# Kernel optimization log

Measured on AMD Instinct MI355X. Metric: run time of the kernel, lower is better.

The kernel has to match this reference:

```python
import jax, jax.numpy as jnp
import numpy as np

PATCH = 16  # SpatialCorrelationSampler patch_size; kernel_size=1, stride=1, dilation_patch=1


def conv3x3(x, w, b):
    # NCHW conv, 3x3, stride 1, padding 1 (matches nn.Conv2d(..., 3, 1, 1))
    y = jax.lax.conv_general_dilated(
        x, w, window_strides=(1, 1), padding=((1, 1), (1, 1)),
        dimension_numbers=('NCHW', 'OIHW', 'NCHW'))
    return y + b[None, :, None, None]


def correlate(f0, f1):
    """SpatialCorrelationSampler(kernel_size=1, patch_size=16, stride=1, padding=0).
    out[b, pi, pj, y, x] = sum_c f0[b,c,y,x] * f1[b,c,y+pi-8, x+pj-8] (zero-padded),
    displacements -8..7 in each axis; no normalization (matches the
    Pytorch-Correlation-extension implementation). Returned flattened to
    [B, PATCH*PATCH, H, W] as the module does via .view."""
    B, C, H, W = f0.shape
    half = PATCH // 2  # 8 -> displacements [-8, 7]
    f1p = jnp.pad(f1, ((0, 0), (0, 0), (half, PATCH - 1 - half), (half, PATCH - 1 - half)))

    def step(_, d):
        pi, pj = d // PATCH, d % PATCH
        f1s = jax.lax.dynamic_slice(f1p, (0, 0, pi, pj), (B, C, H, W))
        return None, jnp.sum(f0 * f1s, axis=1)  # [B, H, W]

    _, corr = jax.lax.scan(step, None, jnp.arange(PATCH * PATCH))  # [256, B, H, W]
    return jnp.transpose(corr, (1, 0, 2, 3))  # [B, 256, H, W]


def setup_inputs() -> dict:
    key = jax.random.key(0)
    ks = jax.random.split(key, 4)
    B, C, H, W = 2, 256, 96, 160  # C == FMAP_DIM (forced: C + 256 + C == 3*C)
    hidden = 256
    f_0 = jax.random.normal(ks[0], (B, C, H, W), jnp.float32)
    f_1 = jax.random.normal(ks[1], (B, C, H, W), jnp.float32)
    W1 = jax.random.normal(ks[2], (hidden, 3 * C, 3, 3), jnp.float32) * 0.02
    b1 = jnp.zeros((hidden,), jnp.float32)
    W2 = jax.random.normal(ks[3], (C, hidden, 3, 3), jnp.float32) * 0.02
    b2 = jnp.zeros((C,), jnp.float32)
    return {"f_0": f_0, "f_1": f_1, "W1": W1, "b1": b1, "W2": W2, "b2": b2}


def reference(f_0, f_1, W1, b1, W2, b2):
    corr = correlate(f_0, f_1)                       # [B, 256, H, W]
    f_cat = jnp.concatenate([f_0, corr, f_1], axis=1)  # [B, 3C, H, W]
    h = jax.nn.relu(conv3x3(f_cat, W1, b1))
    f_1_delta = conv3x3(h, W2, b2)
    return f_1 + f_1_delta
```

## Files before the change

### kernel.cpp

```cpp
#include <hip/hip_runtime.h>
#include <stdint.h>

#define NB 2
#define NC 256
#define NH 96
#define NW 160
#define HP 98
#define WP 162
#define CATC 768
#define P8H 112
#define P8W 176

typedef __bf16 bf16x8 __attribute__((ext_vector_type(8)));
typedef float f32x4 __attribute__((ext_vector_type(4)));

static __device__ __forceinline__ uint16_t f2bf(float f) {
  uint32_t u = __float_as_uint(f);
  return (uint16_t)((u + 0x7fffu + ((u >> 16) & 1u)) >> 16);
}

static __device__ __forceinline__ void gload16(const void* g, void* l) {
  __builtin_amdgcn_global_load_lds(
      (const __attribute__((address_space(1))) uint32_t*)g,
      (__attribute__((address_space(3))) uint32_t*)l, 16, 0, 0);
}

__global__ void __launch_bounds__(256) wprep_kernel(const float* __restrict__ wsrc,
                                                    uint16_t* __restrict__ dst, int cin) {
  int co = blockIdx.x;
  int nb = cin >> 5;
  for (int ci = threadIdx.x; ci < cin; ci += 256) {
    const float* s = wsrc + ((size_t)co * cin + ci) * 9;
    int cb = ci >> 5, cil = ci & 31;
#pragma unroll
    for (int t = 0; t < 9; ++t) {
      dst[(((size_t)t * nb + cb) * 256 + co) * 32 + cil] = f2bf(s[t]);
    }
  }
}

__global__ void __launch_bounds__(256) transpose_kernel(const float* __restrict__ f0,
                                                        const float* __restrict__ f1,
                                                        uint16_t* __restrict__ fcat,
                                                        uint16_t* __restrict__ f1p8) {
  __shared__ float tile[32][33];
  int tid = threadIdx.x;
  int tx = tid & 31, ty = tid >> 5;
  int xb = blockIdx.x;
  int y = blockIdx.y;
  int z = blockIdx.z;
  int b = z >> 4, which = (z >> 3) & 1, cb = z & 7;
  const float* src = which ? f1 : f0;
  int x0 = xb * 32;
#pragma unroll
  for (int j = 0; j < 4; ++j) {
    int c = cb * 32 + ty + j * 8;
    tile[ty + j * 8][tx] = src[((size_t)(b * NC + c) * NH + y) * NW + x0 + tx];
  }
  __syncthreads();
#pragma unroll
  for (int j = 0; j < 4; ++j) {
    int lx = ty + j * 8;
    int x = x0 + lx;
    int c = cb * 32 + tx;
    uint16_t v = f2bf(tile[tx][lx]);
    size_t base = ((size_t)(b * HP + y + 1) * WP + (x + 1)) * CATC;
    if (which == 0) {
      fcat[base + c] = v;
    } else {
      fcat[base + 512 + c] = v;
      f1p8[((size_t)(b * P8H + y + 8) * P8W + (x + 8)) * NC + c] = v;
    }
  }
}

__global__ void __launch_bounds__(256) corr_kernel(const uint16_t* __restrict__ fcat,
                                                   const uint16_t* __restrict__ f1p8,
                                                   uint16_t* __restrict__ fout) {
  int tid = threadIdx.x;
  int lane = tid & 63, w = tid >> 6;
  int lr = lane & 15, lk = lane >> 4;
  int lin = blockIdx.x;
  int wid = (lin & 7) * 120 + (lin >> 3);
  int y = wid % 96, xt = wid / 96;
  int b = blockIdx.y;
  int x0 = xt * 16;

  bf16x8 af[8];
  const uint16_t* abase = fcat + ((size_t)(b * HP + y + 1) * WP + (x0 + lr + 1)) * CATC + lk * 8;
#pragma unroll
  for (int kk = 0; kk < 8; ++kk) af[kk] = *(const bf16x8*)(abase + kk * 32);

  for (int g = 0; g < 4; ++g) {
    int pi = g * 4 + w;
    const uint16_t* bbase =
        f1p8 + ((size_t)(b * P8H + y + pi) * P8W + x0) * NC + lk * 8;
    bf16x8 bf0[8], bf1[8];
#pragma unroll
    for (int kk = 0; kk < 8; ++kk) {
      bf0[kk] = *(const bf16x8*)(bbase + (size_t)lr * NC + kk * 32);
      bf1[kk] = *(const bf16x8*)(bbase + (size_t)(16 + lr) * NC + kk * 32);
    }
    f32x4 acc0 = (f32x4){0.f, 0.f, 0.f, 0.f};
    f32x4 acc1 = (f32x4){0.f, 0.f, 0.f, 0.f};
#pragma unroll
    for (int kk = 0; kk < 8; ++kk) {
      acc0 = __builtin_amdgcn_mfma_f32_16x16x32_bf16(af[kk], bf0[kk], acc0, 0, 0, 0);
      acc1 = __builtin_amdgcn_mfma_f32_16x16x32_bf16(af[kk], bf1[kk], acc1, 0, 0, 0);
    }
    size_t orow = ((size_t)(b * HP + y + 1) * WP + (x0 + 1)) * CATC + 256 + (size_t)pi * 16;
#pragma unroll
    for (int j = 0; j < 4; ++j) {
      int xl = lk * 4 + j;
      int pj0 = lr - xl;
      if (pj0 >= 0) fout[orow + (size_t)xl * CATC + pj0] = f2bf(acc0[j]);
      int pj1 = 16 + lr - xl;
      if (pj1 < 16) fout[orow + (size_t)xl * CATC + pj1] = f2bf(acc1[j]);
    }
  }
}

__global__ __launch_bounds__(512, 2) void conv1_kernel(const uint16_t* __restrict__ fcat,
                                                       const uint16_t* __restrict__ wp,
                                                       const float* __restrict__ bias,
                                                       uint16_t* __restrict__ hbuf) {
  constexpr int CBS = 24, NT = 9 * CBS;
  __shared__ __align__(16) uint16_t As[3][128 * 32];
  int tid = threadIdx.x;
  int w = tid >> 6, lane = tid & 63;
  int lr = lane & 15, lk = lane >> 4;
  int wr = w >> 2, wc = w & 3;

  int orig = blockIdx.x;
  int swz = (orig & 7) * 30 + (orig >> 3);
  int b = swz / 120, rem = swz % 120;
  int xt = rem / 12, yt = rem % 12;
  int x0 = xt * 16, y0 = yt * 8;

  int sr = w * 16 + (lane >> 2);
  int scp = lane & 3;
  int sy = y0 + (sr >> 4), sx = x0 + (sr & 15);
  uint16_t* lds0 = &As[0][0] + sr * 32 + scp * 8;

  float bv[4];
#pragma unroll
  for (int n = 0; n < 4; ++n) bv[n] = bias[wc * 64 + n * 16 + lr];

  f32x4 acc[4][4];
#pragma unroll
  for (int m = 0; m < 4; ++m)
#pragma unroll
    for (int n = 0; n < 4; ++n) acc[m][n] = (f32x4){0.f, 0.f, 0.f, 0.f};

#define STAGE1(kt, buf)                                                                   \
  {                                                                                       \
    int t_ = (kt) / CBS, cb_ = (kt) - t_ * CBS;                                           \
    int dy_ = t_ / 3, dx_ = t_ - dy_ * 3;                                                 \
    const uint16_t* g_ =                                                                  \
        fcat + ((size_t)(b * HP + sy + dy_) * WP + (sx + dx_)) * CATC + cb_ * 32 + scp * 8; \
    gload16(g_, lds0 + (buf)*4096);                                                       \
  }

#define LOADB1(dst, kt)                                                       \
  {                                                                           \
    const uint16_t* s_ = wp + ((size_t)(kt)*256 + wc * 64 + lr) * 32 + lk * 8; \
    _Pragma("unroll") for (int n_ = 0; n_ < 4; ++n_) dst[n_] =                \
        *(const bf16x8*)(s_ + (size_t)n_ * 16 * 32);                          \
  }

  bf16x8 bcur[4], bnext[4];
  STAGE1(0, 0);
  STAGE1(1, 1);
  LOADB1(bcur, 0);
  asm volatile("s_waitcnt vmcnt(5)" ::: "memory");
  __builtin_amdgcn_s_barrier();

  for (int kt = 0; kt < NT; ++kt) {
    int nkt = kt + 2 < NT ? kt + 2 : NT - 1;
    STAGE1(nkt, (kt + 2) % 3);
    int bkt = kt + 1 < NT ? kt + 1 : NT - 1;
    LOADB1(bnext, bkt);
    const uint16_t* a = &As[kt % 3][0];
    bf16x8 af[4];
#pragma unroll
    for (int m = 0; m < 4; ++m)
      af[m] = *(const bf16x8*)(a + (wr * 64 + m * 16 + lr) * 32 + lk * 8);
#pragma unroll
    for (int m = 0; m < 4; ++m)
#pragma unroll
      for (int n = 0; n < 4; ++n)
        acc[m][n] = __builtin_amdgcn_mfma_f32_16x16x32_bf16(af[m], bcur[n], acc[m][n], 0, 0, 0);
#pragma unroll
    for (int n = 0; n < 4; ++n) bcur[n] = bnext[n];
    asm volatile("s_waitcnt vmcnt(5)" ::: "memory");
    __builtin_amdgcn_s_barrier();
  }

#pragma unroll
  for (int m = 0; m < 4; ++m) {
#pragma unroll
    for (int j = 0; j < 4; ++j) {
      int px = wr * 64 + m * 16 + lk * 4 + j;
      int py = px >> 4, pxx = px & 15;
      size_t base = ((size_t)(b * HP + y0 + py + 1) * WP + (x0 + pxx + 1)) * NC;
#pragma unroll
      for (int n = 0; n < 4; ++n) {
        float v = acc[m][n][j] + bv[n];
        v = v > 0.f ? v : 0.f;
        hbuf[base + wc * 64 + n * 16 + lr] = f2bf(v);
      }
    }
  }
#undef STAGE1
#undef LOADB1
}

__global__ __launch_bounds__(512, 2) void conv2_kernel(const uint16_t* __restrict__ hbuf,
                                                       const uint16_t* __restrict__ wp,
                                                       const float* __restrict__ bias,
                                                       const float* __restrict__ f1,
                                                       float* __restrict__ out) {
  constexpr int CBS = 8, NT = 72;
  __shared__ __align__(16) uint16_t Ws[3][256 * 32];
  int tid = threadIdx.x;
  int w = tid >> 6, lane = tid & 63;
  int lr = lane & 15, lk = lane >> 4;
  int wq = w & 3;
  int wph = w >> 2;

  int orig = blockIdx.x;
  int swz = (orig & 7) * 30 + (orig >> 3);
  int b = swz / 120, rem = swz % 120;
  int xt = rem / 12, yt = rem % 12;
  int x0 = xt * 16, y0 = yt * 8;

  int scp = lane & 3;

  float bv[4][4];
#pragma unroll
  for (int m = 0; m < 4; ++m)
#pragma unroll
    for (int j = 0; j < 4; ++j) bv[m][j] = bias[wq * 64 + m * 16 + lk * 4 + j];

  f32x4 acc[4][4];
#pragma unroll
  for (int m = 0; m < 4; ++m)
#pragma unroll
    for (int n = 0; n < 4; ++n) acc[m][n] = (f32x4){0.f, 0.f, 0.f, 0.f};

#define STAGE2(kt, buf)                                                        \
  {                                                                            \
    const uint16_t* g_ = wp + ((size_t)(kt)*256) * 32;                         \
    _Pragma("unroll") for (int j_ = 0; j_ < 2; ++j_) {                         \
      int r_ = w * 32 + j_ * 16 + (lane >> 2);                                 \
      gload16(g_ + r_ * 32 + scp * 8, &Ws[buf][0] + r_ * 32 + scp * 8);        \
    }                                                                          \
  }

#define LOADX2(dst, kt)                                                                     \
  {                                                                                         \
    int t_ = (kt) >> 3, cb_ = (kt)&7;                                                       \
    int dy_ = t_ / 3, dx_ = t_ - dy_ * 3;                                                   \
    _Pragma("unroll") for (int n_ = 0; n_ < 4; ++n_) {                                      \
      const uint16_t* g_ = hbuf +                                                           \
          ((size_t)(b * HP + y0 + wph * 4 + n_ + dy_) * WP + (x0 + lr + dx_)) * NC +        \
          cb_ * 32 + lk * 8;                                                                \
      dst[n_] = *(const bf16x8*)g_;                                                         \
    }                                                                                       \
  }

  bf16x8 xcur[4], xnext[4];
  STAGE2(0, 0);
  STAGE2(1, 1);
  LOADX2(xcur, 0);
  asm volatile("s_waitcnt vmcnt(6)" ::: "memory");
  __builtin_amdgcn_s_barrier();

  for (int kt = 0; kt < NT; ++kt) {
    int nkt = kt + 2 < NT ? kt + 2 : NT - 1;
    STAGE2(nkt, (kt + 2) % 3);
    int bkt = kt + 1 < NT ? kt + 1 : NT - 1;
    LOADX2(xnext, bkt);
    const uint16_t* a = &Ws[kt % 3][0];
    bf16x8 af[4];
#pragma unroll
    for (int m = 0; m < 4; ++m)
      af[m] = *(const bf16x8*)(a + (wq * 64 + m * 16 + lr) * 32 + lk * 8);
#pragma unroll
    for (int m = 0; m < 4; ++m)
#pragma unroll
      for (int n = 0; n < 4; ++n)
        acc[m][n] = __builtin_amdgcn_mfma_f32_16x16x32_bf16(af[m], xcur[n], acc[m][n], 0, 0, 0);
#pragma unroll
    for (int n = 0; n < 4; ++n) xcur[n] = xnext[n];
    asm volatile("s_waitcnt vmcnt(6)" ::: "memory");
    __builtin_amdgcn_s_barrier();
  }

#pragma unroll
  for (int m = 0; m < 4; ++m) {
#pragma unroll
    for (int j = 0; j < 4; ++j) {
      int co = wq * 64 + m * 16 + lk * 4 + j;
#pragma unroll
      for (int n = 0; n < 4; ++n) {
        int y = y0 + wph * 4 + n;
        size_t idx = ((size_t)(b * NC + co) * NH + y) * NW + x0 + lr;
        out[idx] = acc[m][n][j] + bv[m][j] + f1[idx];
      }
    }
  }
#undef STAGE2
#undef LOADX2
}

extern "C" void kernel_launch(void* const* d_in, const int* in_sizes, int n_in,
                              void* d_out, int out_size, void* d_ws, size_t ws_size,
                              hipStream_t stream) {
  (void)in_sizes; (void)n_in; (void)out_size; (void)ws_size;
  const float* f0 = (const float*)d_in[0];
  const float* f1 = (const float*)d_in[1];
  const float* W1 = (const float*)d_in[2];
  const float* b1 = (const float*)d_in[3];
  const float* W2 = (const float*)d_in[4];
  const float* b2 = (const float*)d_in[5];
  float* out = (float*)d_out;

  char* ws = (char*)d_ws;
  size_t s_fcat = (size_t)NB * HP * WP * CATC * 2;
  size_t s_f1p8 = (size_t)NB * P8H * P8W * NC * 2;
  size_t s_h = (size_t)NB * HP * WP * NC * 2;
  size_t s_bp1 = (size_t)9 * 24 * 256 * 32 * 2;
  uint16_t* fcat = (uint16_t*)ws;
  uint16_t* f1p8 = (uint16_t*)(ws + s_fcat);
  uint16_t* hbuf = (uint16_t*)(ws + s_fcat + s_f1p8);
  uint16_t* bp1 = (uint16_t*)(ws + s_fcat + s_f1p8 + s_h);
  uint16_t* bp2 = (uint16_t*)(ws + s_fcat + s_f1p8 + s_h + s_bp1);

  hipMemsetAsync(fcat, 0, s_fcat, stream);
  hipMemsetAsync(f1p8, 0, s_f1p8, stream);
  hipMemsetAsync(hbuf, 0, s_h, stream);

  wprep_kernel<<<256, 256, 0, stream>>>(W1, bp1, 768);
  wprep_kernel<<<256, 256, 0, stream>>>(W2, bp2, 256);
  transpose_kernel<<<dim3(5, 96, 32), 256, 0, stream>>>(f0, f1, fcat, f1p8);
  corr_kernel<<<dim3(960, 2), 256, 0, stream>>>(fcat, f1p8, fcat);
  conv1_kernel<<<240, 512, 0, stream>>>(fcat, bp1, b1, hbuf);
  conv2_kernel<<<240, 512, 0, stream>>>(hbuf, bp2, b2, f1, out);
}
```

Measured before the change: 432.7 us.

## XOR-swizzle LDS tiles and double-buffer register operands in both conv GEMMs

Both implicit-GEMM conv kernels now store their shared-memory tiles with an XOR swizzle on the 16-byte chunk index. The global source address is permuted and the fragment reads use the matching swizzled offset, which is meant to cut LDS bank conflicts on the bf16x8 loads. The main loops are unrolled by two with two alternating register buffers for the directly loaded operand, and each step computes on the current stage before issuing the next loads. This removes the per-iteration register copies, but issuing loads after the MFMAs may hide less memory latency, and the prologue now waits for all outstanding loads.

Measured after the change: 427.5 us. No clear change (-1.2%).

```diff
diff --git a/kernel.cpp b/kernel.cpp
--- a/kernel.cpp
+++ b/kernel.cpp
@@ -139,8 +139,10 @@
 
   int sr = w * 16 + (lane >> 2);
   int scp = lane & 3;
+  int cg = scp ^ ((sr >> 1) & 3);
   int sy = y0 + (sr >> 4), sx = x0 + (sr & 15);
   uint16_t* lds0 = &As[0][0] + sr * 32 + scp * 8;
+  int cswz = (lk ^ ((lr >> 1) & 3)) * 8;
 
   float bv[4];
 #pragma unroll
@@ -152,48 +154,59 @@
 #pragma unroll
     for (int n = 0; n < 4; ++n) acc[m][n] = (f32x4){0.f, 0.f, 0.f, 0.f};
 
-#define STAGE1(kt, buf)                                                                   \
-  {                                                                                       \
-    int t_ = (kt) / CBS, cb_ = (kt) - t_ * CBS;                                           \
-    int dy_ = t_ / 3, dx_ = t_ - dy_ * 3;                                                 \
-    const uint16_t* g_ =                                                                  \
-        fcat + ((size_t)(b * HP + sy + dy_) * WP + (sx + dx_)) * CATC + cb_ * 32 + scp * 8; \
-    gload16(g_, lds0 + (buf)*4096);                                                       \
-  }
-
-#define LOADB1(dst, kt)                                                       \
-  {                                                                           \
+#define STAGE1(kt, buf)                                                                     \
+  {                                                                                         \
+    int t_ = (kt) / CBS, cb_ = (kt) - t_ * CBS;                                             \
+    int dy_ = t_ / 3, dx_ = t_ - dy_ * 3;                                                   \
+    const uint16_t* g_ =                                                                    \
+        fcat + ((size_t)(b * HP + sy + dy_) * WP + (sx + dx_)) * CATC + cb_ * 32 + cg * 8;  \
+    gload16(g_, lds0 + (buf)*4096);                                                         \
+  }
+
+#define LOADB1(dst, kt)                                                        \
+  {                                                                            \
     const uint16_t* s_ = wp + ((size_t)(kt)*256 + wc * 64 + lr) * 32 + lk * 8; \
-    _Pragma("unroll") for (int n_ = 0; n_ < 4; ++n_) dst[n_] =                \
-        *(const bf16x8*)(s_ + (size_t)n_ * 16 * 32);                          \
-  }
-
-  bf16x8 bcur[4], bnext[4];
+    _Pragma("unroll") for (int n_ = 0; n_ < 4; ++n_) dst[n_] =                 \
+        *(const bf16x8*)(s_ + (size_t)n_ * 512);                               \
+  }
+
+#define MFMA1(bufidx, breg)                                                          \
+  {                                                                                  \
+    const uint16_t* a_ = &As[bufidx][0];                                             \
+    bf16x8 af[4];                                                                    \
+    _Pragma("unroll") for (int m_ = 0; m_ < 4; ++m_) af[m_] =                        \
+        *(const bf16x8*)(a_ + (wr * 64 + m_ * 16 + lr) * 32 + cswz);                 \
+    _Pragma("unroll") for (int m_ = 0; m_ < 4; ++m_)                                 \
+        _Pragma("unroll") for (int n_ = 0; n_ < 4; ++n_) acc[m_][n_] =               \
+            __builtin_amdgcn_mfma_f32_16x16x32_bf16(af[m_], breg[n_], acc[m_][n_],   \
+                                                    0, 0, 0);                        \
+  }
+
+  bf16x8 b0[4], b1[4];
   STAGE1(0, 0);
+  LOADB1(b0, 0);
   STAGE1(1, 1);
-  LOADB1(bcur, 0);
-  asm volatile("s_waitcnt vmcnt(5)" ::: "memory");
+  LOADB1(b1, 1);
+  asm volatile("s_waitcnt vmcnt(0)" ::: "memory");
   __builtin_amdgcn_s_barrier();
 
-  for (int kt = 0; kt < NT; ++kt) {
-    int nkt = kt + 2 < NT ? kt + 2 : NT - 1;
-    STAGE1(nkt, (kt + 2) % 3);
-    int bkt = kt + 1 < NT ? kt + 1 : NT - 1;
-    LOADB1(bnext, bkt);
-    const uint16_t* a = &As[kt % 3][0];
-    bf16x8 af[4];
-#pragma unroll
-    for (int m = 0; m < 4; ++m)
-      af[m] = *(const bf16x8*)(a + (wr * 64 + m * 16 + lr) * 32 + lk * 8);
-#pragma unroll
-    for (int m = 0; m < 4; ++m)
-#pragma unroll
-      for (int n = 0; n < 4; ++n)
-        acc[m][n] = __builtin_amdgcn_mfma_f32_16x16x32_bf16(af[m], bcur[n], acc[m][n], 0, 0, 0);
-#pragma unroll
-    for (int n = 0; n < 4; ++n) bcur[n] = bnext[n];
-    asm volatile("s_waitcnt vmcnt(5)" ::: "memory");
-    __builtin_amdgcn_s_barrier();
+  for (int kt = 0; kt < NT; kt += 2) {
+    {
+      MFMA1(kt % 3, b0);
+      int nk = (kt + 2 < NT) ? kt + 2 : NT - 1;
+      STAGE1(nk, (kt + 2) % 3);
+      LOADB1(b0, nk);
+      asm volatile("s_waitcnt vmcnt(5)" ::: "memory");
+      __builtin_amdgcn_s_barrier();
+    }
+    {
+      MFMA1((kt + 1) % 3, b1);
+      int nk = (kt + 3 < NT) ? kt + 3 : NT - 1;
+      STAGE1(nk, (kt + 3) % 3);
+      LOADB1(b1, nk);
+      asm volatile("s_waitcnt vmcnt(5)" ::: "memory");
+      __builtin_amdgcn_s_barrier();
+    }
   }
 
 #pragma unroll
@@ -213,6 +226,7 @@
   }
 #undef STAGE1
 #undef LOADB1
+#undef MFMA1
 }
 
 __global__ __launch_bounds__(512, 2) void conv2_kernel(const uint16_t* __restrict__ hbuf,
@@ -220,7 +234,7 @@
                                                        const float* __restrict__ bias,
                                                        const float* __restrict__ f1,
                                                        float* __restrict__ out) {
-  constexpr int CBS = 8, NT = 72;
+  constexpr int NT = 72;
   __shared__ __align__(16) uint16_t Ws[3][256 * 32];
   int tid = threadIdx.x;
   int w = tid >> 6, lane = tid & 63;
@@ -235,6 +249,8 @@
   int x0 = xt * 16, y0 = yt * 8;
 
   int scp = lane & 3;
+  int srw0 = w * 32 + (lane >> 2);
+  int cswz = (lk ^ ((lr >> 1) & 3)) * 8;
 
   float bv[4][4];
 #pragma unroll
@@ -248,13 +264,15 @@
 #pragma unroll
     for (int n = 0; n < 4; ++n) acc[m][n] = (f32x4){0.f, 0.f, 0.f, 0.f};
 
-#define STAGE2(kt, buf)                                                        \
-  {                                                                            \
-    const uint16_t* g_ = wp + ((size_t)(kt)*256) * 32;                         \
-    _Pragma("unroll") for (int j_ = 0; j_ < 2; ++j_) {                         \
-      int r_ = w * 32 + j_ * 16 + (lane >> 2);                                 \
-      gload16(g_ + r_ * 32 + scp * 8, &Ws[buf][0] + r_ * 32 + scp * 8);        \
-    }                                                                          \
+#define STAGE2(kt, buf)                                                         \
+  {                                                                             \
+    const uint16_t* g_ = wp + ((size_t)(kt)*256) * 32;                          \
+    _Pragma("unroll") for (int j_ = 0; j_ < 2; ++j_) {                          \
+      int r_ = srw0 + j_ * 16;                                                  \
+      int cg_ = scp ^ ((r_ >> 1) & 3);                                          \
+      gload16(g_ + (size_t)r_ * 32 + cg_ * 8,                                   \
+              &Ws[buf][0] + r_ * 32 + scp * 8);                                 \
+    }                                                                           \
   }
 
 #define LOADX2(dst, kt)                                                                     \
@@ -269,32 +287,43 @@
     }                                                                                       \
   }
 
-  bf16x8 xcur[4], xnext[4];
+#define MFMA2(bufidx, xreg)                                                          \
+  {                                                                                  \
+    const uint16_t* a_ = &Ws[bufidx][0];                                             \
+    bf16x8 aw[4];                                                                    \
+    _Pragma("unroll") for (int m_ = 0; m_ < 4; ++m_) aw[m_] =                        \
+        *(const bf16x8*)(a_ + (wq * 64 + m_ * 16 + lr) * 32 + cswz);                 \
+    _Pragma("unroll") for (int m_ = 0; m_ < 4; ++m_)                                 \
+        _Pragma("unroll") for (int n_ = 0; n_ < 4; ++n_) acc[m_][n_] =               \
+            __builtin_amdgcn_mfma_f32_16x16x32_bf16(aw[m_], xreg[n_], acc[m_][n_],   \
+                                                    0, 0, 0);                        \
+  }
+
+  bf16x8 x0r[4], x1r[4];
   STAGE2(0, 0);
+  LOADX2(x0r, 0);
   STAGE2(1, 1);
-  LOADX2(xcur, 0);
-  asm volatile("s_waitcnt vmcnt(6)" ::: "memory");
+  LOADX2(x1r, 1);
+  asm volatile("s_waitcnt vmcnt(0)" ::: "memory");
   __builtin_amdgcn_s_barrier();
 
-  for (int kt = 0; kt < NT; ++kt) {
-    int nkt = kt + 2 < NT ? kt + 2 : NT - 1;
-    STAGE2(nkt, (kt + 2) % 3);
-    int bkt = kt + 1 < NT ? kt + 1 : NT - 1;
-    LOADX2(xnext, bkt);
-    const uint16_t* a = &Ws[kt % 3][0];
-    bf16x8 af[4];
-#pragma unroll
-    for (int m = 0; m < 4; ++m)
-      af[m] = *(const bf16x8*)(a + (wq * 64 + m * 16 + lr) * 32 + lk * 8);
-#pragma unroll
-    for (int m = 0; m < 4; ++m)
-#pragma unroll
-      for (int n = 0; n < 4; ++n)
-        acc[m][n] = __builtin_amdgcn_mfma_f32_16x16x32_bf16(af[m], xcur[n], acc[m][n], 0, 0, 0);
-#pragma unroll
-    for (int n = 0; n < 4; ++n) xcur[n] = xnext[n];
-    asm volatile("s_waitcnt vmcnt(6)" ::: "memory");
-    __builtin_amdgcn_s_barrier();
+  for (int kt = 0; kt < NT; kt += 2) {
+    {
+      MFMA2(kt % 3, x0r);
+      int nk = (kt + 2 < NT) ? kt + 2 : NT - 1;
+      STAGE2(nk, (kt + 2) % 3);
+      LOADX2(x0r, nk);
+      asm volatile("s_waitcnt vmcnt(6)" ::: "memory");
+      __builtin_amdgcn_s_barrier();
+    }
+    {
+      MFMA2((kt + 1) % 3, x1r);
+      int nk = (kt + 3 < NT) ? kt + 3 : NT - 1;
+      STAGE2(nk, (kt + 3) % 3);
+      LOADX2(x1r, nk);
+      asm volatile("s_waitcnt vmcnt(6)" ::: "memory");
+      __builtin_amdgcn_s_barrier();
+    }
   }
 
 #pragma unroll
@@ -312,6 +341,7 @@
   }
 #undef STAGE2
 #undef LOADX2
+#undef MFMA2
 }
 
 extern "C" void kernel_launch(void* const* d_in, const int* in_sizes, int n_in,
```
